# Performance work log

Measured on AMD Instinct MI355X. Metric: run time of the kernel, lower is better.

## Reference

```python
import jax, jax.numpy as jnp
import numpy as np

EPSILON = 1e-10
NUM_STATES = 16
EPS_POT = 1.0
DIFFUSION = 3
N_NODES = 100000
N_UND_EDGES = 1600000
FEAT_DIM = 128


def setup_inputs() -> dict:
    key = jax.random.key(0)
    k1, k2, k3, k4 = jax.random.split(key, 4)
    features = jax.random.normal(k1, (N_NODES, FEAT_DIM), dtype=jnp.float32)
    W = jax.random.normal(k2, (FEAT_DIM, NUM_STATES), dtype=jnp.float32) * 0.05
    u = jax.random.randint(k3, (N_UND_EDGES,), 0, N_NODES)
    v = jax.random.randint(k4, (N_UND_EDGES,), 0, N_NODES)
    # directed edge lists: each undirected edge appears in both directions
    src_nodes = jnp.concatenate([u, v])
    dst_nodes = jnp.concatenate([v, u])
    e = jnp.arange(N_UND_EDGES)
    rev_edges = jnp.concatenate([e + N_UND_EDGES, e])  # index of reversed edge
    return {
        "features": features,
        "W": W,
        "src_nodes": src_nodes,
        "dst_nodes": dst_nodes,
        "rev_edges": rev_edges,
    }


def reference(features, W, src_nodes, dst_nodes, rev_edges):
    num_dir_edges = src_nodes.shape[0]
    potential = jnp.exp(jnp.eye(NUM_STATES, dtype=features.dtype) * EPS_POT)
    # classifier: linear + softmax -> probability priors [N, S]
    priors = jax.nn.softmax(features @ W, axis=1)
    log_priors = jnp.log(jnp.maximum(priors, EPSILON))

    beliefs = priors
    messages = jnp.full((num_dir_edges, NUM_STATES), 1.0 / NUM_STATES,
                        dtype=features.dtype)
    for _ in range(DIFFUSION):
        # message update: gather-divide-matmul-renormalize
        new_beliefs = beliefs[src_nodes]          # [2E, S]
        rev_messages = messages[rev_edges]        # [2E, S]
        new_msgs = (new_beliefs / rev_messages) @ potential
        messages = new_msgs / new_msgs.sum(axis=1, keepdims=True)
        # belief update: scatter-add of log messages, then softmax
        log_msgs = jnp.log(jnp.maximum(messages, EPSILON))
        log_b = log_priors.at[dst_nodes].add(log_msgs)
        beliefs = jax.nn.softmax(log_b, axis=1)
    return (priors, beliefs)
```

## Files before the change

kernel.cpp:

```cpp
#include <hip/hip_runtime.h>
#include <hip/hip_fp16.h>

#define NSTATES 16

static __device__ __forceinline__ float4 ld4(const float* p) {
    return *reinterpret_cast<const float4*>(p);
}

struct h4 { __half2 a, b; };

static __device__ __forceinline__ float4 ldh4(const __half* p) {
    h4 v = *reinterpret_cast<const h4*>(p);
    float2 fa = __half22float2(v.a);
    float2 fb = __half22float2(v.b);
    return make_float4(fa.x, fa.y, fb.x, fb.y);
}
static __device__ __forceinline__ void sth4(__half* p, float4 f) {
    h4 v;
    v.a = __floats2half2_rn(f.x, f.y);
    v.b = __floats2half2_rn(f.z, f.w);
    *reinterpret_cast<h4*>(p) = v;
}

__global__ void priors_kernel(const float* __restrict__ feat,
                              const float* __restrict__ W,
                              float* __restrict__ priors_out,
                              float* __restrict__ beliefs,
                              float* __restrict__ log_priors,
                              int n_nodes)
{
    __shared__ float Wl[128 * NSTATES];
    for (int i = threadIdx.x; i < 128 * NSTATES; i += blockDim.x)
        Wl[i] = W[i];
    __syncthreads();

    long long gid = (long long)blockIdx.x * blockDim.x + threadIdx.x;
    int node = (int)(gid >> 4);
    if (node >= n_nodes) return;
    int s = (int)(gid & 15);

    const float4* f4 = reinterpret_cast<const float4*>(feat + (size_t)node * 128);
    float acc = 0.f;
#pragma unroll
    for (int i = 0; i < 32; ++i) {
        float4 f = f4[i];
        acc = fmaf(f.x, Wl[(i * 4 + 0) * NSTATES + s], acc);
        acc = fmaf(f.y, Wl[(i * 4 + 1) * NSTATES + s], acc);
        acc = fmaf(f.z, Wl[(i * 4 + 2) * NSTATES + s], acc);
        acc = fmaf(f.w, Wl[(i * 4 + 3) * NSTATES + s], acc);
    }
    float mx = acc;
#pragma unroll
    for (int off = 1; off < 16; off <<= 1)
        mx = fmaxf(mx, __shfl_xor(mx, off, 64));
    float ex = expf(acc - mx);
    float sm = ex;
#pragma unroll
    for (int off = 1; off < 16; off <<= 1)
        sm += __shfl_xor(sm, off, 64);
    float p = ex / sm;

    size_t idx = (size_t)node * NSTATES + s;
    priors_out[idx] = p;
    beliefs[idx]    = p;
    log_priors[idx] = logf(fmaxf(p, 1e-10f));
}

__global__ void rank_kernel(const int* __restrict__ dst, int* __restrict__ cnt,
                            int* __restrict__ r, int n)
{
    int i = blockIdx.x * blockDim.x + threadIdx.x;
    if (i < n) r[i] = atomicAdd(&cnt[dst[i]], 1);
}

__global__ void scan1_kernel(const int* __restrict__ cnt,
                             int* __restrict__ row_ptr,
                             int* __restrict__ bsum, int n)
{
    int base = blockIdx.x * 1024;
    int t = threadIdx.x;
    int i0 = base + t * 4;
    int a0 = (i0 + 0 < n) ? cnt[i0 + 0] : 0;
    int a1 = (i0 + 1 < n) ? cnt[i0 + 1] : 0;
    int a2 = (i0 + 2 < n) ? cnt[i0 + 2] : 0;
    int a3 = (i0 + 3 < n) ? cnt[i0 + 3] : 0;
    int sl = a0 + a1 + a2 + a3;

    int lane = t & 63, wid = t >> 6;
    int v = sl;
#pragma unroll
    for (int off = 1; off < 64; off <<= 1) {
        int tv = __shfl_up(v, off, 64);
        if (lane >= off) v += tv;
    }
    __shared__ int wtot[4], woff[4];
    if (lane == 63) wtot[wid] = v;
    __syncthreads();
    if (t == 0) {
        int a = 0;
        for (int w = 0; w < 4; ++w) { woff[w] = a; a += wtot[w]; }
        bsum[blockIdx.x] = a;
    }
    __syncthreads();
    int excl = woff[wid] + (v - sl);
    if (i0 + 0 < n) row_ptr[i0 + 0] = excl;
    if (i0 + 1 < n) row_ptr[i0 + 1] = excl + a0;
    if (i0 + 2 < n) row_ptr[i0 + 2] = excl + a0 + a1;
    if (i0 + 3 < n) row_ptr[i0 + 3] = excl + a0 + a1 + a2;
}

__global__ void scan2_kernel(int* __restrict__ bsum, int nb)
{
    __shared__ int run;
    int lane = threadIdx.x;
    if (lane == 0) run = 0;
    __syncthreads();
    for (int b = 0; b < nb; b += 64) {
        int i = b + lane;
        int x = (i < nb) ? bsum[i] : 0;
        int v = x;
#pragma unroll
        for (int off = 1; off < 64; off <<= 1) {
            int tv = __shfl_up(v, off, 64);
            if (lane >= off) v += tv;
        }
        int excl = run + v - x;
        if (i < nb) bsum[i] = excl;
        __syncthreads();
        if (lane == 63) run = excl + x;
        __syncthreads();
    }
}

__global__ void scan3_kernel(int* __restrict__ row_ptr,
                             const int* __restrict__ bsum, int n, int total)
{
    int i = blockIdx.x * blockDim.x + threadIdx.x;
    if (i < n) row_ptr[i] += bsum[i >> 10];
    if (i == 0) row_ptr[n] = total;
}

__global__ void slots_kernel(const int* __restrict__ dst,
                             const int* __restrict__ row_ptr,
                             int* __restrict__ r, int n)
{
    int i = blockIdx.x * blockDim.x + threadIdx.x;
    if (i < n) r[i] = row_ptr[dst[i]] + r[i];
}

template <bool FIRST>
__global__ void edge_kernel(const float* __restrict__ beliefs,
                            __half* __restrict__ messages,
                            const int* __restrict__ src,
                            const int* __restrict__ dst,
                            const int* __restrict__ slot_of,
                            int n_pairs)
{
    long long gid = (long long)blockIdx.x * blockDim.x + threadIdx.x;
    int p = (int)(gid >> 2);
    if (p >= n_pairs) return;
    int sub = (int)(gid & 3);

    int u  = src[p];
    int v  = dst[p];
    int sF = slot_of[p];
    int sR = slot_of[p + n_pairs];

    const float EM1  = 1.7182818284590452354f;
    const float SUMF = 17.718281828459045235f;

    float4 bu = ld4(beliefs + (size_t)u * NSTATES + sub * 4);
    float4 bv = ld4(beliefs + (size_t)v * NSTATES + sub * 4);

    float4 tf, tr;
    if (FIRST) {
        tf = make_float4(bu.x * 16.f, bu.y * 16.f, bu.z * 16.f, bu.w * 16.f);
        tr = make_float4(bv.x * 16.f, bv.y * 16.f, bv.z * 16.f, bv.w * 16.f);
    } else {
        float4 mf = ldh4(messages + (size_t)sF * NSTATES + sub * 4);
        float4 mr = ldh4(messages + (size_t)sR * NSTATES + sub * 4);
        tf = make_float4(bu.x / mr.x, bu.y / mr.y, bu.z / mr.z, bu.w / mr.w);
        tr = make_float4(bv.x / mf.x, bv.y / mf.y, bv.z / mf.z, bv.w / mf.w);
    }

    float sf = (tf.x + tf.y) + (tf.z + tf.w);
    float sr = (tr.x + tr.y) + (tr.z + tr.w);
    sf += __shfl_xor(sf, 1, 64);
    sf += __shfl_xor(sf, 2, 64);
    sr += __shfl_xor(sr, 1, 64);
    sr += __shfl_xor(sr, 2, 64);

    float invf = 1.0f / (SUMF * sf);
    float invr = 1.0f / (SUMF * sr);

    float4 nf, nr;
    nf.x = fmaf(EM1, tf.x, sf) * invf;
    nf.y = fmaf(EM1, tf.y, sf) * invf;
    nf.z = fmaf(EM1, tf.z, sf) * invf;
    nf.w = fmaf(EM1, tf.w, sf) * invf;
    nr.x = fmaf(EM1, tr.x, sr) * invr;
    nr.y = fmaf(EM1, tr.y, sr) * invr;
    nr.z = fmaf(EM1, tr.z, sr) * invr;
    nr.w = fmaf(EM1, tr.w, sr) * invr;

    sth4(messages + (size_t)sF * NSTATES + sub * 4, nf);
    sth4(messages + (size_t)sR * NSTATES + sub * 4, nr);
}

__global__ void belief_kernel(const __half* __restrict__ messages,
                              const int* __restrict__ row_ptr,
                              const float* __restrict__ log_priors,
                              float* __restrict__ beliefs,
                              int n_nodes)
{
    long long gid = (long long)blockIdx.x * blockDim.x + threadIdx.x;
    int node = (int)(gid >> 6);
    if (node >= n_nodes) return;
    int lane = threadIdx.x & 63;
    int cp   = lane & 7;
    int rg   = lane >> 3;

    int start = row_ptr[node];
    int end   = row_ptr[node + 1];

    float acc0 = 0.f, acc1 = 0.f;
    for (int row = start + rg; row < end; row += 8) {
        __half2 m2 = *reinterpret_cast<const __half2*>(
            messages + (size_t)row * NSTATES + cp * 2);
        float2 f = __half22float2(m2);
        acc0 += logf(fmaxf(f.x, 1e-10f));
        acc1 += logf(fmaxf(f.y, 1e-10f));
    }
#pragma unroll
    for (int off = 8; off < 64; off <<= 1) {
        acc0 += __shfl_xor(acc0, off, 64);
        acc1 += __shfl_xor(acc1, off, 64);
    }

    float2 lp = *reinterpret_cast<const float2*>(
        log_priors + (size_t)node * NSTATES + cp * 2);
    float lb0 = acc0 + lp.x;
    float lb1 = acc1 + lp.y;

    float mx = fmaxf(lb0, lb1);
#pragma unroll
    for (int off = 1; off < 8; off <<= 1)
        mx = fmaxf(mx, __shfl_xor(mx, off, 64));
    float e0 = expf(lb0 - mx);
    float e1 = expf(lb1 - mx);
    float sm = e0 + e1;
#pragma unroll
    for (int off = 1; off < 8; off <<= 1)
        sm += __shfl_xor(sm, off, 64);
    float inv = 1.0f / sm;

    if (rg == 0) {
        float2 b = make_float2(e0 * inv, e1 * inv);
        *reinterpret_cast<float2*>(beliefs + (size_t)node * NSTATES + cp * 2) = b;
    }
}

extern "C" void kernel_launch(void* const* d_in, const int* in_sizes, int n_in,
                              void* d_out, int out_size, void* d_ws, size_t ws_size,
                              hipStream_t stream)
{
    const float* feat = (const float*)d_in[0];
    const float* W    = (const float*)d_in[1];
    const int*   src  = (const int*)d_in[2];
    const int*   dst  = (const int*)d_in[3];

    int n_nodes = in_sizes[0] / 128;
    int n_dir   = in_sizes[2];
    int n_pairs = n_dir / 2;

    float* out         = (float*)d_out;
    float* priors_out  = out;
    float* beliefs     = out + (size_t)n_nodes * NSTATES;

    size_t NN16 = (size_t)n_nodes * NSTATES;
    size_t ME   = (size_t)n_dir * NSTATES;

    float*  ws         = (float*)d_ws;
    float*  log_priors = ws;
    __half* messages   = (__half*)(log_priors + NN16);
    int*    slot_of    = (int*)(messages + ME);
    int*    row_ptr    = slot_of + n_dir;
    int*    cnt        = row_ptr + n_nodes + 1;
    int*    bsum       = cnt + n_nodes;

    const int BLK = 256;
    int nb    = (n_nodes + 1023) / 1024;
    int grid1 = (int)((NN16 + BLK - 1) / BLK);
    int gridE = (int)(((size_t)n_pairs * 4 + BLK - 1) / BLK);
    int gridH = (n_dir + BLK - 1) / BLK;
    int gridN = (n_nodes + BLK - 1) / BLK;
    int gridB = (int)(((size_t)n_nodes * 64 + BLK - 1) / BLK);

    hipMemsetAsync(cnt, 0, (size_t)n_nodes * sizeof(int), stream);
    rank_kernel<<<gridH, BLK, 0, stream>>>(dst, cnt, slot_of, n_dir);
    scan1_kernel<<<nb, 256, 0, stream>>>(cnt, row_ptr, bsum, n_nodes);
    scan2_kernel<<<1, 64, 0, stream>>>(bsum, nb);
    scan3_kernel<<<gridN, BLK, 0, stream>>>(row_ptr, bsum, n_nodes, n_dir);
    slots_kernel<<<gridH, BLK, 0, stream>>>(dst, row_ptr, slot_of, n_dir);

    priors_kernel<<<grid1, BLK, 0, stream>>>(feat, W, priors_out, beliefs,
                                             log_priors, n_nodes);

    edge_kernel<true><<<gridE, BLK, 0, stream>>>(beliefs, messages, src, dst,
                                                 slot_of, n_pairs);
    belief_kernel<<<gridB, BLK, 0, stream>>>(messages, row_ptr, log_priors,
                                             beliefs, n_nodes);

    edge_kernel<false><<<gridE, BLK, 0, stream>>>(beliefs, messages, src, dst,
                                                  slot_of, n_pairs);
    belief_kernel<<<gridB, BLK, 0, stream>>>(messages, row_ptr, log_priors,
                                             beliefs, n_nodes);

    edge_kernel<false><<<gridE, BLK, 0, stream>>>(beliefs, messages, src, dst,
                                                  slot_of, n_pairs);
    belief_kernel<<<gridB, BLK, 0, stream>>>(messages, row_ptr, log_priors,
                                             beliefs, n_nodes);
}
```

Baseline: 815.7 us.

## Replace global-atomic edge ranking with LDS-partitioned histogram and column scan

The CSR build used to rank edges with global atomics on per-node counters and then add row offsets in a second pass. It now splits edges into 32 chunks and nodes into 4 partitions, builds per-chunk node histograms with LDS atomics, and column-scans them into per-chunk offsets. A final pass recomputes each edge's slot from the row pointer, the chunk offset and a local LDS rank. The aim is to replace contended global atomics with shared-memory ones, at the cost of a large per-chunk count buffer, reading dst twice per pass, and only 128 blocks of 1024 threads each.

Measured after the change: 760.5 us. 6.8% less time.

```diff
diff --git a/kernel.cpp b/kernel.cpp
--- a/kernel.cpp
+++ b/kernel.cpp
@@ -2,6 +2,8 @@
 #include <hip/hip_fp16.h>
 
 #define NSTATES 16
+#define P_PART 4
+#define C_CHUNK 32
 
 static __device__ __forceinline__ float4 ld4(const float* p) {
     return *reinterpret_cast<const float4*>(p);
@@ -66,11 +68,41 @@
     log_priors[idx] = logf(fmaxf(p, 1e-10f));
 }
 
-__global__ void rank_kernel(const int* __restrict__ dst, int* __restrict__ cnt,
-                            int* __restrict__ r, int n)
-{
-    int i = blockIdx.x * blockDim.x + threadIdx.x;
-    if (i < n) r[i] = atomicAdd(&cnt[dst[i]], 1);
+__global__ void __launch_bounds__(1024) hist1_kernel(
+    const int* __restrict__ dst, int* __restrict__ percount,
+    int n, int n_nodes, int bins, int chunk)
+{
+    extern __shared__ int lh[];
+    int c = blockIdx.x & (C_CHUNK - 1);
+    int p = blockIdx.x / C_CHUNK;
+    int base = p * bins;
+    for (int i = threadIdx.x; i < bins; i += 1024) lh[i] = 0;
+    __syncthreads();
+    int lo = c * chunk, hi = min(lo + chunk, n);
+    for (int i = lo + threadIdx.x; i < hi; i += 1024) {
+        int d = dst[i] - base;
+        if ((unsigned)d < (unsigned)bins) atomicAdd(&lh[d], 1);
+    }
+    __syncthreads();
+    int lim = min(bins, n_nodes - base);
+    int* out = percount + (size_t)c * n_nodes + base;
+    for (int i = threadIdx.x; i < lim; i += 1024) out[i] = lh[i];
+}
+
+__global__ void colscan_kernel(int* __restrict__ percount,
+                               int* __restrict__ cnt, int n_nodes)
+{
+    int v = blockIdx.x * blockDim.x + threadIdx.x;
+    if (v >= n_nodes) return;
+    int acc = 0;
+#pragma unroll
+    for (int c = 0; c < C_CHUNK; ++c) {
+        size_t idx = (size_t)c * n_nodes + v;
+        int x = percount[idx];
+        percount[idx] = acc;
+        acc += x;
+    }
+    cnt[v] = acc;
 }
 
 __global__ void scan1_kernel(const int* __restrict__ cnt,
@@ -140,12 +172,27 @@
     if (i == 0) row_ptr[n] = total;
 }
 
-__global__ void slots_kernel(const int* __restrict__ dst,
-                             const int* __restrict__ row_ptr,
-                             int* __restrict__ r, int n)
-{
-    int i = blockIdx.x * blockDim.x + threadIdx.x;
-    if (i < n) r[i] = row_ptr[dst[i]] + r[i];
+__global__ void __launch_bounds__(1024) slot3_kernel(
+    const int* __restrict__ dst, const int* __restrict__ row_ptr,
+    const int* __restrict__ percount, int* __restrict__ slot_of,
+    int n, int n_nodes, int bins, int chunk)
+{
+    extern __shared__ int lh[];
+    int c = blockIdx.x & (C_CHUNK - 1);
+    int p = blockIdx.x / C_CHUNK;
+    int base = p * bins;
+    for (int i = threadIdx.x; i < bins; i += 1024) lh[i] = 0;
+    __syncthreads();
+    int lo = c * chunk, hi = min(lo + chunk, n);
+    const int* pc = percount + (size_t)c * n_nodes;
+    for (int i = lo + threadIdx.x; i < hi; i += 1024) {
+        int d = dst[i];
+        int ld = d - base;
+        if ((unsigned)ld < (unsigned)bins) {
+            int lr = atomicAdd(&lh[ld], 1);
+            slot_of[i] = row_ptr[d] + pc[d] + lr;
+        }
+    }
 }
 
 template <bool FIRST>
@@ -287,21 +334,25 @@
     int*    row_ptr    = slot_of + n_dir;
     int*    cnt        = row_ptr + n_nodes + 1;
     int*    bsum       = cnt + n_nodes;
+    int*    percount   = bsum + ((n_nodes + 1023) / 1024) + 1;
 
     const int BLK = 256;
     int nb    = (n_nodes + 1023) / 1024;
+    int bins  = (n_nodes + P_PART - 1) / P_PART;
+    int chunk = (n_dir + C_CHUNK - 1) / C_CHUNK;
     int grid1 = (int)((NN16 + BLK - 1) / BLK);
     int gridE = (int)(((size_t)n_pairs * 4 + BLK - 1) / BLK);
-    int gridH = (n_dir + BLK - 1) / BLK;
     int gridN = (n_nodes + BLK - 1) / BLK;
     int gridB = (int)(((size_t)n_nodes * 64 + BLK - 1) / BLK);
 
-    hipMemsetAsync(cnt, 0, (size_t)n_nodes * sizeof(int), stream);
-    rank_kernel<<<gridH, BLK, 0, stream>>>(dst, cnt, slot_of, n_dir);
+    hist1_kernel<<<P_PART * C_CHUNK, 1024, bins * sizeof(int), stream>>>(
+        dst, percount, n_dir, n_nodes, bins, chunk);
+    colscan_kernel<<<gridN, BLK, 0, stream>>>(percount, cnt, n_nodes);
     scan1_kernel<<<nb, 256, 0, stream>>>(cnt, row_ptr, bsum, n_nodes);
     scan2_kernel<<<1, 64, 0, stream>>>(bsum, nb);
     scan3_kernel<<<gridN, BLK, 0, stream>>>(row_ptr, bsum, n_nodes, n_dir);
-    slots_kernel<<<gridH, BLK, 0, stream>>>(dst, row_ptr, slot_of, n_dir);
+    slot3_kernel<<<P_PART * C_CHUNK, 1024, bins * sizeof(int), stream>>>(
+        dst, row_ptr, percount, slot_of, n_dir, n_nodes, bins, chunk);
 
     priors_kernel<<<grid1, BLK, 0, stream>>>(feat, W, priors_out, beliefs,
                                              log_priors, n_nodes);
```
